# Kernel optimization log

Hardware: AMD Instinct MI355X
Metric: run time of the kernel (lower is better)

The kernel has to match this reference:

```python
import jax, jax.numpy as jnp
import numpy as np

NUM_JOINTS = 24
PARENTS = np.array([-1, 0, 0, 0, 1, 2, 3, 4, 5, 6, 7, 8, 9, 9, 9, 12, 13, 14, 16, 17, 18, 19, 20, 21])
SENSOR_IDX = np.array([0, 4, 5, 15, 18, 19])          # pelvis, knees, head, elbows (6 IMUs)
IGNORED_IDX = np.array([7, 8, 10, 11, 20, 21, 22, 23])  # ankles, feet, wrists, hands
REDUCED_IDX = np.array([1, 2, 3, 6, 9, 12, 13, 14, 16, 17])  # 10 reduced joints
IGNORED_PARENTS = PARENTS[IGNORED_IDX]


def rotation_6d_to_matrix(d6):
    # pytorch3d convention: rows b1, b2, b3
    a1, a2 = d6[..., :3], d6[..., 3:]
    b1 = a1 / jnp.linalg.norm(a1, axis=-1, keepdims=True)
    b2 = a2 - jnp.sum(b1 * a2, axis=-1, keepdims=True) * b1
    b2 = b2 / jnp.linalg.norm(b2, axis=-1, keepdims=True)
    b3 = jnp.cross(b1, b2)
    return jnp.stack([b1, b2, b3], axis=-2)


def matrix_to_quaternion(m):
    m00, m01, m02 = m[..., 0, 0], m[..., 0, 1], m[..., 0, 2]
    m10, m11, m12 = m[..., 1, 0], m[..., 1, 1], m[..., 1, 2]
    m20, m21, m22 = m[..., 2, 0], m[..., 2, 1], m[..., 2, 2]
    q_abs = jnp.sqrt(jnp.maximum(jnp.stack([
        1.0 + m00 + m11 + m22,
        1.0 + m00 - m11 - m22,
        1.0 - m00 + m11 - m22,
        1.0 - m00 - m11 + m22], axis=-1), 0.0))
    quat_by_rijk = jnp.stack([
        jnp.stack([q_abs[..., 0] ** 2, m21 - m12, m02 - m20, m10 - m01], axis=-1),
        jnp.stack([m21 - m12, q_abs[..., 1] ** 2, m10 + m01, m02 + m20], axis=-1),
        jnp.stack([m02 - m20, m10 + m01, q_abs[..., 2] ** 2, m12 + m21], axis=-1),
        jnp.stack([m10 - m01, m20 + m02, m21 + m12, q_abs[..., 3] ** 2], axis=-1),
    ], axis=-2)
    quat_candidates = quat_by_rijk / (2.0 * jnp.maximum(q_abs[..., None], 0.1))
    idx = jnp.argmax(q_abs, axis=-1)
    return jnp.take_along_axis(quat_candidates, idx[..., None, None], axis=-2)[..., 0, :]


def quaternion_to_axis_angle(q):
    norms = jnp.linalg.norm(q[..., 1:], axis=-1, keepdims=True)
    half_angles = jnp.arctan2(norms, q[..., :1])
    angles = 2.0 * half_angles
    small = jnp.abs(angles) < 1e-6
    safe_angles = jnp.where(small, 1.0, angles)
    sin_half_over_angle = jnp.where(small, 0.5 - angles * angles / 48.0,
                                    jnp.sin(half_angles) / safe_angles)
    return q[..., 1:] / sin_half_over_angle


def matrix_to_axis_angle(m):
    return quaternion_to_axis_angle(matrix_to_quaternion(m))


def setup_inputs() -> dict:
    key = jax.random.key(0)
    k1, k2 = jax.random.split(key)
    B, T = 1024, 256
    glb_reduced_6d = jax.random.normal(k1, (B, T, len(REDUCED_IDX), 6), dtype=jnp.float32)
    orientation_6d = jax.random.normal(k2, (B, T, len(SENSOR_IDX), 6), dtype=jnp.float32)
    return {"glb_reduced_6d": glb_reduced_6d, "orientation_6d": orientation_6d}


def reference(glb_reduced_6d, orientation_6d):
    B, T = glb_reduced_6d.shape[:2]
    BT = B * T
    dtype = glb_reduced_6d.dtype
    glb6 = glb_reduced_6d.reshape(BT, len(REDUCED_IDX), 6)
    ori6 = orientation_6d.reshape(BT, len(SENSOR_IDX), 6)

    orientation = rotation_6d_to_matrix(ori6)          # [BT, 6, 3, 3]
    root = orientation[:, 0]                           # [BT, 3, 3]
    reduced_rot = rotation_6d_to_matrix(glb6)          # [BT, 10, 3, 3]

    # _reduced_glb_6d_to_full_glb_mat
    reduced_glb = jnp.einsum('bij,brjk->brik', root, reduced_rot)
    ori_glb = orientation.at[:, 1:].set(jnp.einsum('bij,bsjk->bsik', root, orientation[:, 1:]))
    eye = jnp.eye(3, dtype=dtype)
    full = jnp.broadcast_to(eye, (BT, NUM_JOINTS, 3, 3))
    full = full.at[:, REDUCED_IDX].set(reduced_glb)
    full = full.at[:, SENSOR_IDX].set(ori_glb)
    # torch advanced-index assignment: RHS gathered from pre-update values
    full = full.at[:, IGNORED_IDX].set(full[:, IGNORED_PARENTS])

    # _global2local: local_i = R_parent(i)^T @ R_i (vectorized over static parent gather)
    parent_rot = full[:, PARENTS[1:]]                  # [BT, 23, 3, 3]
    local_rest = jnp.einsum('bjki,bjkl->bjil', parent_rot, full[:, 1:])
    local = jnp.concatenate([full[:, :1], local_rest], axis=1)
    local = local.at[:, IGNORED_IDX].set(eye)

    pose_aa = matrix_to_axis_angle(local)              # [BT, 24, 3]
    return pose_aa.reshape(B, T, NUM_JOINTS, 3)
```

## Files before the change

### kernel.cpp

```cpp
#include <hip/hip_runtime.h>
#include <math.h>


__device__ __forceinline__ void rot6d(const float* __restrict__ d, float M[3][3]) {
    float a1x = d[0], a1y = d[1], a1z = d[2];
    float a2x = d[3], a2y = d[4], a2z = d[5];
    float r1 = __builtin_amdgcn_rsqf(a1x * a1x + a1y * a1y + a1z * a1z);
    float b1x = a1x * r1, b1y = a1y * r1, b1z = a1z * r1;
    float dt = b1x * a2x + b1y * a2y + b1z * a2z;
    float c2x = a2x - dt * b1x, c2y = a2y - dt * b1y, c2z = a2z - dt * b1z;
    float r2 = __builtin_amdgcn_rsqf(c2x * c2x + c2y * c2y + c2z * c2z);
    float b2x = c2x * r2, b2y = c2y * r2, b2z = c2z * r2;
    float b3x = b1y * b2z - b1z * b2y;
    float b3y = b1z * b2x - b1x * b2z;
    float b3z = b1x * b2y - b1y * b2x;
    M[0][0] = b1x; M[0][1] = b1y; M[0][2] = b1z;
    M[1][0] = b2x; M[1][1] = b2y; M[1][2] = b2z;
    M[2][0] = b3x; M[2][1] = b3y; M[2][2] = b3z;
}

__device__ __forceinline__ void matmul(const float A[3][3], const float B[3][3], float C[3][3]) {
#pragma unroll
    for (int i = 0; i < 3; ++i)
#pragma unroll
        for (int j = 0; j < 3; ++j)
            C[i][j] = A[i][0] * B[0][j] + A[i][1] * B[1][j] + A[i][2] * B[2][j];
}

__device__ __forceinline__ void matTmul(const float A[3][3], const float B[3][3], float C[3][3]) {
#pragma unroll
    for (int i = 0; i < 3; ++i)
#pragma unroll
        for (int j = 0; j < 3; ++j)
            C[i][j] = A[0][i] * B[0][j] + A[1][i] * B[1][j] + A[2][i] * B[2][j];
}

__device__ __forceinline__ float atan2_pos(float y, float x) {
    float ax = fabsf(x);
    float mx = fmaxf(y, ax);
    float mn = fminf(y, ax);
    float a = mn * __builtin_amdgcn_rcpf(mx);
    float s = a * a;
    float p = -0.0040540580f;
    p = fmaf(p, s, 0.0218612288f);
    p = fmaf(p, s, -0.0559098861f);
    p = fmaf(p, s, 0.0964200441f);
    p = fmaf(p, s, -0.1390853351f);
    p = fmaf(p, s, 0.1994653599f);
    p = fmaf(p, s, -0.3332985605f);
    p = fmaf(p, s, 0.9999993329f);
    float r = p * a;
    r = (y > ax) ? (1.5707963268f - r) : r;
    r = (x < 0.f) ? (3.1415926536f - r) : r;
    return r;
}

__device__ __forceinline__ void mat2aa(const float m[3][3], float* __restrict__ outp) {
    float m00 = m[0][0], m01 = m[0][1], m02 = m[0][2];
    float m10 = m[1][0], m11 = m[1][1], m12 = m[1][2];
    float m20 = m[2][0], m21 = m[2][1], m22 = m[2][2];
    float t0 = fmaxf(1.f + m00 + m11 + m22, 0.f);
    float t1 = fmaxf(1.f + m00 - m11 - m22, 0.f);
    float t2 = fmaxf(1.f - m00 + m11 - m22, 0.f);
    float t3 = fmaxf(1.f - m00 - m11 + m22, 0.f);
    int idx = 0;
    float bt = t0;
    if (t1 > bt) { bt = t1; idx = 1; }
    if (t2 > bt) { bt = t2; idx = 2; }
    if (t3 > bt) { bt = t3; idx = 3; }
    float best = __builtin_amdgcn_sqrtf(bt);
    float s1 = m21 - m12, s2 = m02 - m20, s3 = m10 - m01;
    float p1 = m10 + m01, p2 = m02 + m20, p3 = m12 + m21;
    float w = (idx == 0) ? bt : (idx == 1) ? s1 : (idx == 2) ? s2 : s3;
    float x = (idx == 0) ? s1 : (idx == 1) ? bt : (idx == 2) ? p1 : p2;
    float y = (idx == 0) ? s2 : (idx == 1) ? p1 : (idx == 2) ? bt : p3;
    float z = (idx == 0) ? s3 : (idx == 1) ? p2 : (idx == 2) ? p3 : bt;
    float inv = 0.5f * __builtin_amdgcn_rcpf(fmaxf(best, 0.1f));
    w *= inv; x *= inv; y *= inv; z *= inv;
    float n = __builtin_amdgcn_sqrtf(x * x + y * y + z * z);
    float half = atan2_pos(n, w);
    float angle = 2.f * half;
    float inv_sh = (angle < 1e-6f) ? 2.f : angle * __builtin_amdgcn_rcpf(n);
    outp[0] = x * inv_sh;
    outp[1] = y * inv_sh;
    outp[2] = z * inv_sh;
}

__global__ __launch_bounds__(256) void pose_kernel(const float* __restrict__ glb,
                                                   const float* __restrict__ ori,
                                                   float* __restrict__ out, int BT) {
    int tid = blockIdx.x * 256 + threadIdx.x;
    int e = tid >> 4;
    if (e >= BT) return;
    int l = tid & 15;

    const float* __restrict__ ge = glb + (size_t)e * 60;
    const float* __restrict__ oe = ori + (size_t)e * 36;
    float* __restrict__ oute = out + (size_t)e * 72;

    const unsigned long long OUT3_LO = 0x1B120F0C09060300ULL;
    const unsigned long long OUT3_HI = 0x393633302D2A2724ULL;
    const unsigned long long SRCJ_LO = 0x0403121102010010ULL;
    const unsigned long long SRCJ_HI = 0x1514090813070605ULL;
    const unsigned long long PR1_LO  = 0x0403020100000000ULL;
    const unsigned long long PR1_HI  = 0x0A09080706050505ULL;
    const unsigned long long IGN3    = 0x45423F3C211E1815ULL;

    int sh = (l & 7) * 8;
    int out3 = (int)(((l < 8 ? OUT3_LO : OUT3_HI) >> sh) & 0xFF);
    int srcj = (int)(((l < 8 ? SRCJ_LO : SRCJ_HI) >> sh) & 0xFF);
    int pr1  = (int)(((l < 8 ? PR1_LO  : PR1_HI)  >> sh) & 0xFF);

    float root[3][3];
    rot6d(oe, root);

    const float* pj = (srcj & 0x10) ? (oe + (srcj & 0xF) * 6) : (ge + (srcj & 0xF) * 6);
    float T[3][3], Fj[3][3];
    rot6d(pj, T);
    matmul(root, T, Fj);

    const float* pp = pr1 ? (ge + (pr1 - 1) * 6) : oe;
    float Fp[3][3];
    rot6d(pp, T);
    matmul(root, T, Fp);

    float P[3][3];
#pragma unroll
    for (int i = 0; i < 3; ++i)
#pragma unroll
        for (int j = 0; j < 3; ++j)
            P[i][j] = pr1 ? Fp[i][j] : root[i][j];

    float L[3][3];
    matTmul(P, Fj, L);
#pragma unroll
    for (int i = 0; i < 3; ++i)
#pragma unroll
        for (int j = 0; j < 3; ++j)
            L[i][j] = (l == 0) ? root[i][j] : L[i][j];

    mat2aa(L, oute + out3);

    if (l < 8) {
        int z = (int)((IGN3 >> sh) & 0xFF);
        float* zp = oute + z;
        zp[0] = 0.f; zp[1] = 0.f; zp[2] = 0.f;
    }
}

extern "C" void kernel_launch(void* const* d_in, const int* in_sizes, int n_in,
                              void* d_out, int out_size, void* d_ws, size_t ws_size,
                              hipStream_t stream) {
    const float* glb = (const float*)d_in[0];
    const float* ori = (const float*)d_in[1];
    float* out = (float*)d_out;
    int BT = in_sizes[0] / 60;
    long long threads = (long long)BT * 16;
    int block = 256;
    int grid = (int)((threads + block - 1) / block);
    pose_kernel<<<grid, block, 0, stream>>>(glb, ori, out, BT);
}
```

Before: 152.9 us.

## Cancel root rotation algebraically and fetch parent rotation via lane shuffle

Each lane now builds only its own 6D-to-matrix rotation and reads its parent's matrix from a neighbouring lane with a width-16 shuffle. Because local = (R_root·T_p)^T(R_root·T_j) = T_p^T·T_j for an orthonormal root, the root multiply is dropped entirely. Lanes for the pelvis and the root's children use their own matrix directly. Inputs are loaded as float2 pairs. This cuts per-lane work from three rot6d conversions plus two matmuls to one conversion and a shuffle. The cost is cross-lane traffic and small floating-point differences from dropping the root product.

```diff
diff --git a/kernel.cpp b/kernel.cpp
--- a/kernel.cpp
+++ b/kernel.cpp
@@ -2,9 +2,9 @@
 #include <math.h>
 
 
-__device__ __forceinline__ void rot6d(const float* __restrict__ d, float M[3][3]) {
-    float a1x = d[0], a1y = d[1], a1z = d[2];
-    float a2x = d[3], a2y = d[4], a2z = d[5];
+__device__ __forceinline__ void rot6d_v(float2 u0, float2 u1, float2 u2, float M[3][3]) {
+    float a1x = u0.x, a1y = u0.y, a1z = u1.x;
+    float a2x = u1.y, a2y = u2.x, a2z = u2.y;
     float r1 = __builtin_amdgcn_rsqf(a1x * a1x + a1y * a1y + a1z * a1z);
     float b1x = a1x * r1, b1y = a1y * r1, b1z = a1z * r1;
     float dt = b1x * a2x + b1y * a2y + b1z * a2z;
@@ -17,14 +17,6 @@
     M[0][0] = b1x; M[0][1] = b1y; M[0][2] = b1z;
     M[1][0] = b2x; M[1][1] = b2y; M[1][2] = b2z;
     M[2][0] = b3x; M[2][1] = b3y; M[2][2] = b3z;
-}
-
-__device__ __forceinline__ void matmul(const float A[3][3], const float B[3][3], float C[3][3]) {
-#pragma unroll
-    for (int i = 0; i < 3; ++i)
-#pragma unroll
-        for (int j = 0; j < 3; ++j)
-            C[i][j] = A[i][0] * B[0][j] + A[i][1] * B[1][j] + A[i][2] * B[2][j];
 }
 
 __device__ __forceinline__ void matTmul(const float A[3][3], const float B[3][3], float C[3][3]) {
@@ -102,42 +94,37 @@
     const unsigned long long OUT3_HI = 0x393633302D2A2724ULL;
     const unsigned long long SRCJ_LO = 0x0403121102010010ULL;
     const unsigned long long SRCJ_HI = 0x1514090813070605ULL;
-    const unsigned long long PR1_LO  = 0x0403020100000000ULL;
-    const unsigned long long PR1_HI  = 0x0A09080706050505ULL;
+    const unsigned long long PL_LO   = 0x0603020100000000ULL;
+    const unsigned long long PL_HI   = 0x0D0C0A0908070707ULL;
     const unsigned long long IGN3    = 0x45423F3C211E1815ULL;
 
     int sh = (l & 7) * 8;
     int out3 = (int)(((l < 8 ? OUT3_LO : OUT3_HI) >> sh) & 0xFF);
     int srcj = (int)(((l < 8 ? SRCJ_LO : SRCJ_HI) >> sh) & 0xFF);
-    int pr1  = (int)(((l < 8 ? PR1_LO  : PR1_HI)  >> sh) & 0xFF);
+    int pl   = (int)(((l < 8 ? PL_LO   : PL_HI)   >> sh) & 0xFF);
 
-    float root[3][3];
-    rot6d(oe, root);
+    const float* src = (srcj & 0x10) ? (oe + (srcj & 15) * 6) : (ge + (srcj & 15) * 6);
+    const float2* s2 = (const float2*)src;
+    float2 u0 = s2[0], u1 = s2[1], u2 = s2[2];
 
-    const float* pj = (srcj & 0x10) ? (oe + (srcj & 0xF) * 6) : (ge + (srcj & 0xF) * 6);
-    float T[3][3], Fj[3][3];
-    rot6d(pj, T);
-    matmul(root, T, Fj);
+    float X[3][3];
+    rot6d_v(u0, u1, u2, X);
 
-    const float* pp = pr1 ? (ge + (pr1 - 1) * 6) : oe;
-    float Fp[3][3];
-    rot6d(pp, T);
-    matmul(root, T, Fp);
+    float Xp[3][3];
+    {
+        const float* xf = &X[0][0];
+        float* pf = &Xp[0][0];
+#pragma unroll
+        for (int k = 0; k < 9; ++k) pf[k] = __shfl(xf[k], pl, 16);
+    }
 
-    float P[3][3];
+    float L[3][3];
+    matTmul(Xp, X, L);
 #pragma unroll
     for (int i = 0; i < 3; ++i)
 #pragma unroll
         for (int j = 0; j < 3; ++j)
-            P[i][j] = pr1 ? Fp[i][j] : root[i][j];
-
-    float L[3][3];
-    matTmul(P, Fj, L);
-#pragma unroll
-    for (int i = 0; i < 3; ++i)
-#pragma unroll
-        for (int j = 0; j < 3; ++j)
-            L[i][j] = (l == 0) ? root[i][j] : L[i][j];
+            L[i][j] = (l < 4) ? X[i][j] : L[i][j];
 
     mat2aa(L, oute + out3);
 
```

Result: no change. 150.9 us (median of 2 runs) (-1.3%).
